# Performance work log

Measured on AMD Instinct MI355X. Metric: run time of the kernel, lower is better.

The kernel has to match this reference:

```python
import jax, jax.numpy as jnp
import numpy as np

H = 1024
VOCAB = 32000


def setup_inputs() -> dict:
    key = jax.random.key(0)
    ks = jax.random.split(key, 16)
    N, B, T = 32, 64, 400
    s = 1.0 / np.sqrt(H)
    inp = {
        "input_seq": jax.random.randint(ks[0], (N, B), 0, VOCAB),
        "last_hidden": jax.random.normal(ks[1], (1, B, H), jnp.float32),
        "encoder_outputs": jax.random.normal(ks[2], (T, B, H), jnp.float32),
        "encoderB_outputs": jax.random.normal(ks[3], (T, B, H), jnp.float32),
        # parameters
        "emb": jax.random.normal(ks[4], (VOCAB, H), jnp.float32),
        "W_ih": jax.random.uniform(ks[5], (3 * H, H), jnp.float32, -s, s),
        "W_hh": jax.random.uniform(ks[6], (3 * H, H), jnp.float32, -s, s),
        "b_ih": jax.random.uniform(ks[7], (3 * H,), jnp.float32, -s, s),
        "b_hh": jax.random.uniform(ks[8], (3 * H,), jnp.float32, -s, s),
        "attn_W": jax.random.uniform(ks[9], (H, 2 * H), jnp.float32, -s, s),
        "attn_b": jax.random.uniform(ks[10], (H,), jnp.float32, -s, s),
        "attn_v": jax.random.uniform(ks[11], (H,), jnp.float32, -s, s),
        "concat_W": jax.random.uniform(ks[12], (H, 3 * H), jnp.float32, -s, s),
        "concat_b": jax.random.uniform(ks[13], (H,), jnp.float32, -s, s),
        "out_W": jax.random.uniform(ks[14], (VOCAB, H), jnp.float32, -s, s),
        "out_b": jax.random.uniform(ks[15], (VOCAB,), jnp.float32, -s, s),
    }
    return inp


def _gru(x, h0, W_ih, W_hh, b_ih, b_hh):
    # x: (N,B,H), h0: (B,H). PyTorch GRU cell equations.
    def step(h, x_t):
        gi = x_t @ W_ih.T + b_ih          # (B,3H)
        gh = h @ W_hh.T + b_hh
        i_r, i_z, i_n = jnp.split(gi, 3, axis=-1)
        h_r, h_z, h_n = jnp.split(gh, 3, axis=-1)
        r = jax.nn.sigmoid(i_r + h_r)
        z = jax.nn.sigmoid(i_z + h_z)
        n = jnp.tanh(i_n + r * h_n)
        h_new = (1.0 - z) * n + z * h
        return h_new, h_new
    hN, outs = jax.lax.scan(step, h0, x)
    return outs, hN


def _attention(rnn_out, enc, attn_W, attn_b, v):
    # score(h, e) = (Linear([h; e]) ) . v  -- linear in both, so separable.
    W1, W2 = attn_W[:, :H], attn_W[:, H:]
    u1 = W1.T @ v                         # (H,)
    u2 = W2.T @ v
    bias = attn_b @ v                     # scalar
    a = rnn_out @ u1                      # (N,B)
    c = enc @ u2 + bias                   # (T,B)
    # energies (B,N,T), softmax over T (matches F.softmax on (-1, max_len))
    e = a.T[:, :, None] + c.T[:, None, :]
    w = jax.nn.softmax(e, axis=-1)        # (B,N,T)
    ctx = jnp.einsum('bnt,tbh->nbh', w, enc)  # bmm then transpose(0,1)
    return w, ctx


def reference(input_seq, last_hidden, encoder_outputs, encoderB_outputs,
              emb, W_ih, W_hh, b_ih, b_hh, attn_W, attn_b, attn_v,
              concat_W, concat_b, out_W, out_b):
    x = emb[input_seq]                                   # (N,B,H)
    rnn_out, hN = _gru(x, last_hidden[0], W_ih, W_hh, b_ih, b_hh)
    hidden = hN[None]                                    # (1,B,H)
    uw, u_ctx = _attention(rnn_out, encoder_outputs, attn_W, attn_b, attn_v)
    bw, b_ctx = _attention(rnn_out, encoderB_outputs, attn_W, attn_b, attn_v)
    cat = jnp.concatenate([rnn_out, u_ctx, b_ctx], axis=2)   # (N,B,3H)
    h = jnp.tanh(cat @ concat_W.T + concat_b)
    output = h @ out_W.T + out_b                          # (N,B,VOCAB)
    return output, hidden, uw, bw
```

## Files before the change

kernel.cpp:

```cpp
#include <hip/hip_runtime.h>
#include <cstdint>
#include <cstddef>

namespace {

constexpr int kH  = 1024;
constexpr int kB  = 64;
constexpr int kN  = 32;
constexpr int kT  = 400;
constexpr int kV  = 32000;
constexpr int kM  = kN * kB;
constexpr int k3H = 3 * kH;

typedef _Float16 f16;
typedef _Float16 f16x4 __attribute__((ext_vector_type(4)));
typedef _Float16 f16x8 __attribute__((ext_vector_type(8)));
typedef float    f32x4v __attribute__((ext_vector_type(4)));

__device__ __forceinline__ void gload_lds16(const void* g, void* l) {
  __builtin_amdgcn_global_load_lds((__attribute__((address_space(1))) void*)g,
                                   (__attribute__((address_space(3))) void*)l,
                                   16, 0, 0);
}

__device__ __forceinline__ uint32_t pack_f16x2(f16 lo, f16 hi) {
  union { f16 h[2]; uint32_t u; } c;
  c.h[0] = lo; c.h[1] = hi;
  return c.u;
}


__global__ __launch_bounds__(256)
void pre_kernel(const float* __restrict__ Wih, f16* __restrict__ WihH,
                const float* __restrict__ Whh, f16* __restrict__ WhhH,
                const int* __restrict__ seq, const float* __restrict__ emb,
                f16* __restrict__ Xh, const float* __restrict__ lh,
                f16* __restrict__ HH0,
                const float* __restrict__ attnW, const float* __restrict__ attnB,
                const float* __restrict__ attnV,
                float* __restrict__ u2, float* __restrict__ biasS) {
  const int bid = blockIdx.x, tid = threadIdx.x;
  if (bid < 512) {
    const float* src = (bid < 256) ? Wih : Whh;
    f16* dst = (bid < 256) ? WihH : WhhH;
    constexpr int n4 = k3H * kH / 4;
    for (int i = (bid & 255) * 256 + tid; i < n4; i += 256 * 256) {
      float4 v = reinterpret_cast<const float4*>(src)[i];
      f16x4 o = { (f16)v.x, (f16)v.y, (f16)v.z, (f16)v.w };
      reinterpret_cast<f16x4*>(dst)[i] = o;
    }
  } else if (bid < 640) {
    const int m0 = (bid - 512) * 16;
    for (int k = 0; k < 16; ++k) {
      const int m = m0 + k;
      const int tok = seq[m];
      float4 v = reinterpret_cast<const float4*>(emb + (size_t)tok * kH)[tid];
      f16x4 o = { (f16)v.x, (f16)v.y, (f16)v.z, (f16)v.w };
      reinterpret_cast<f16x4*>(Xh + (size_t)m * kH)[tid] = o;
    }
  } else if (bid < 644) {
    for (int i = (bid - 640) * 256 + tid; i < 16384; i += 1024) {
      float4 v = reinterpret_cast<const float4*>(lh)[i];
      f16x4 o = { (f16)v.x, (f16)v.y, (f16)v.z, (f16)v.w };
      reinterpret_cast<f16x4*>(HH0)[i] = o;
    }
  } else {
    const int item = (bid - 644) * 4 + (tid >> 6);
    const int lane = tid & 63;
    if (item > kH) return;
    float sum = 0.0f;
    if (item < kH) {
      for (int k = lane; k < kH; k += 64)
        sum += attnW[(size_t)k * (2 * kH) + kH + item] * attnV[k];
    } else {
      for (int k = lane; k < kH; k += 64)
        sum += attnB[k] * attnV[k];
    }
    #pragma unroll
    for (int o = 32; o > 0; o >>= 1) sum += __shfl_xor(sum, o);
    if (lane == 0) { if (item < kH) u2[item] = sum; else biasS[0] = sum; }
  }
}


template <int MODE, typename OUT_T>
__global__ __launch_bounds__(256)
void gemm_bt2_kernel(const f16* __restrict__ A, const f16* __restrict__ Bt,
                     const float* __restrict__ bias, OUT_T* __restrict__ C,
                     int M, int N, int K) {
  __shared__ union {
    struct { __align__(16) f16 As[128 * 64]; __align__(16) f16 Bs[128 * 64]; } st;
    float rp32[64][132];
    f16   rp16[128][132];
  } sm;
  int bx, by;
  if (MODE == 2) {
    const int nrow = M >> 7;
    const int cpx  = gridDim.x >> 3;
    const int wgid = (blockIdx.x & 7) * cpx + (blockIdx.x >> 3);
    bx = wgid % nrow;  by = wgid / nrow;
  } else {
    bx = blockIdx.x;  by = blockIdx.y;
  }
  const int tid  = threadIdx.x;
  const int wave = tid >> 6;
  const int lane = tid & 63;
  const int m0 = bx * 128;
  const int n0 = by * 128;
  const int wm = (wave >> 1) * 64;
  const int wn = (wave & 1) * 64;
  const int rsub = lane >> 3;
  const int coff = (lane & 7) * 8;
  f32x4v acc[4][4] = {};
  const int nk = K >> 6;
  for (int kc = 0; kc < nk; ++kc) {
    const f16* Ag = A + (size_t)m0 * K + kc * 64;
    const f16* Bg = Bt + (size_t)n0 * K + kc * 64;
    for (int c = wave; c < 16; c += 4) {
      const int row = c * 8 + rsub;
      gload_lds16(Ag + (size_t)row * K + coff, &sm.st.As[c * 512]);
      gload_lds16(Bg + (size_t)row * K + coff, &sm.st.Bs[c * 512]);
    }
    __syncthreads();
    #pragma unroll
    for (int kk = 0; kk < 2; ++kk) {
      const int ko = kk * 32 + (lane >> 4) * 8;
      f16x8 af[4], bfr[4];
      #pragma unroll
      for (int i = 0; i < 4; ++i) {
        af[i]  = *reinterpret_cast<const f16x8*>(&sm.st.As[(wm + i * 16 + (lane & 15)) * 64 + ko]);
        bfr[i] = *reinterpret_cast<const f16x8*>(&sm.st.Bs[(wn + i * 16 + (lane & 15)) * 64 + ko]);
      }
      #pragma unroll
      for (int mi = 0; mi < 4; ++mi)
        #pragma unroll
        for (int ni = 0; ni < 4; ++ni)
          acc[mi][ni] = __builtin_amdgcn_mfma_f32_16x16x32_f16(af[mi], bfr[ni], acc[mi][ni], 0, 0, 0);
    }
    __syncthreads();
  }
  const int rb = (lane >> 4) * 4;
  const int cb = lane & 15;

  if (MODE == 1) {
    #pragma unroll
    for (int mi = 0; mi < 4; ++mi)
      #pragma unroll
      for (int ni = 0; ni < 4; ++ni) {
        const int col = wn + ni * 16 + cb;
        const float bv = bias[n0 + col];
        #pragma unroll
        for (int r = 0; r < 4; ++r)
          sm.rp16[wm + mi * 16 + rb + r][col] = (f16)tanhf(acc[mi][ni][r] + bv);
      }
    __syncthreads();
    #pragma unroll
    for (int i = 0; i < 8; ++i) {
      const int idx = i * 256 + tid;
      const int row = idx >> 4;
      const int c8  = (idx & 15) * 8;
      f16x8 v = *reinterpret_cast<const f16x8*>(&sm.rp16[row][c8]);
      *reinterpret_cast<f16x8*>(&C[(size_t)(m0 + row) * N + n0 + c8]) = v;
    }
  } else {
    #pragma unroll
    for (int half = 0; half < 2; ++half) {
      __syncthreads();
      if ((wm >> 6) == half) {
        #pragma unroll
        for (int mi = 0; mi < 4; ++mi)
          #pragma unroll
          for (int ni = 0; ni < 4; ++ni) {
            const int col = wn + ni * 16 + cb;
            const float bv = bias[n0 + col];
            #pragma unroll
            for (int r = 0; r < 4; ++r)
              sm.rp32[mi * 16 + rb + r][col] = acc[mi][ni][r] + bv;
          }
      }
      __syncthreads();
      #pragma unroll
      for (int i = 0; i < 8; ++i) {
        const int idx = i * 256 + tid;
        const int row = idx >> 5;
        const int c4  = (idx & 31) * 4;
        f32x4v v = *reinterpret_cast<const f32x4v*>(&sm.rp32[row][c4]);
        float* dst = (float*)&C[(size_t)(m0 + half * 64 + row) * N + n0 + c4];
        if (MODE == 2) __builtin_nontemporal_store(v, reinterpret_cast<f32x4v*>(dst));
        else *reinterpret_cast<f32x4v*>(dst) = v;
      }
    }
  }
}


constexpr int kGruBlks = 64;
constexpr int kAttnBlks = 128;
constexpr int kCvtBlks = 320;
constexpr int kMegaBlks = kGruBlks + kAttnBlks + kCvtBlks;

__global__ __launch_bounds__(256, 1)
void mega_kernel(const f16* __restrict__ Whh, const float* __restrict__ bhh,
                 const float* __restrict__ gi, const float* __restrict__ lh,
                 f16* __restrict__ HHa, f16* __restrict__ HHb,
                 f16* __restrict__ cath, float* __restrict__ hiddenOut,
                 unsigned int* __restrict__ flags,
                 const float* __restrict__ enc0, const float* __restrict__ enc1,
                 const float* __restrict__ u2, const float* __restrict__ biasS,
                 float* __restrict__ uw, float* __restrict__ bw,
                 const float* __restrict__ oW, f16* __restrict__ oWh,
                 const float* __restrict__ cW, f16* __restrict__ cWh) {
  __shared__ union SM {
    float ghp[4][64][52];
    struct { float4 u2s[256]; float srow[kT]; float red[8]; } at;
  } sm;
  const int bid = blockIdx.x;
  const int tid = threadIdx.x;
  const int wave = tid >> 6;
  const int lane = tid & 63;

  if (bid < kGruBlks) {
    const int ln   = lane & 15;
    const int khi  = lane >> 4;
    const int j0   = bid * 16;
    const int kw   = wave * 256;
    const int fm   = tid >> 2;
    const int fc   = (tid & 3) * 4;
    const int myprod = wave * 16 + ln;

    f16x8 bfr[3][8];
    #pragma unroll
    for (int s = 0; s < 3; ++s)
      #pragma unroll
      for (int ks = 0; ks < 8; ++ks)
        bfr[s][ks] = *reinterpret_cast<const f16x8*>(
            &Whh[(size_t)(s * kH + j0 + ln) * kH + kw + ks * 32 + khi * 8]);

    float hreg[4], bR[4], bZ[4], bN[4];
    #pragma unroll
    for (int e = 0; e < 4; ++e) {
      const int j = j0 + fc + e;
      hreg[e] = lh[(size_t)fm * kH + j];
      bR[e] = bhh[j]; bZ[e] = bhh[kH + j]; bN[e] = bhh[2 * kH + j];
    }

    for (int step = 0; step < kN; ++step) {
      const f16* hh  = (step & 1) ? HHb : HHa;
      f16*       hho = (step & 1) ? HHa : HHb;

      float4 giL[3];
      {
        const size_t mm = (size_t)step * kB + fm;
        #pragma unroll
        for (int s = 0; s < 3; ++s)
          giL[s] = *reinterpret_cast<const float4*>(&gi[mm * k3H + s * kH + j0 + fc]);
      }

      if (step > 0) {
        while (true) {
          unsigned int f = __hip_atomic_load(&flags[myprod], __ATOMIC_RELAXED,
                                             __HIP_MEMORY_SCOPE_SYSTEM);
          if (__all(f >= (unsigned int)step)) break;
          __builtin_amdgcn_s_sleep(1);
        }
        __builtin_amdgcn_fence(__ATOMIC_ACQUIRE, "agent");
      }

      f16x8 af[8][4];
      #pragma unroll
      for (int ks = 0; ks < 8; ++ks)
        #pragma unroll
        for (int mi = 0; mi < 4; ++mi)
          af[ks][mi] = *reinterpret_cast<const f16x8*>(
              &hh[(size_t)(mi * 16 + ln) * kH + kw + ks * 32 + khi * 8]);

      f32x4v acc[4][3] = {};
      #pragma unroll
      for (int ks = 0; ks < 8; ++ks)
        #pragma unroll
        for (int mi = 0; mi < 4; ++mi)
          #pragma unroll
          for (int s = 0; s < 3; ++s)
            acc[mi][s] = __builtin_amdgcn_mfma_f32_16x16x32_f16(af[ks][mi], bfr[s][ks], acc[mi][s], 0, 0, 0);

      #pragma unroll
      for (int mi = 0; mi < 4; ++mi)
        #pragma unroll
        for (int s = 0; s < 3; ++s)
          #pragma unroll
          for (int r = 0; r < 4; ++r)
            sm.ghp[wave][mi * 16 + khi * 4 + r][s * 16 + ln] = acc[mi][s][r];
      __syncthreads();

      float4 gr4 = {0,0,0,0}, gz4 = {0,0,0,0}, gn4 = {0,0,0,0};
      #pragma unroll
      for (int w = 0; w < 4; ++w) {
        float4 a = *reinterpret_cast<const float4*>(&sm.ghp[w][fm][fc]);
        float4 b = *reinterpret_cast<const float4*>(&sm.ghp[w][fm][16 + fc]);
        float4 c = *reinterpret_cast<const float4*>(&sm.ghp[w][fm][32 + fc]);
        gr4.x += a.x; gr4.y += a.y; gr4.z += a.z; gr4.w += a.w;
        gz4.x += b.x; gz4.y += b.y; gz4.z += b.z; gz4.w += b.w;
        gn4.x += c.x; gn4.y += c.y; gn4.z += c.z; gn4.w += c.w;
      }
      float hv[4];
      const float* grp = &gr4.x; const float* gzp = &gz4.x; const float* gnp = &gn4.x;
      const float* g0 = &giL[0].x; const float* g1 = &giL[1].x; const float* g2 = &giL[2].x;
      #pragma unroll
      for (int e = 0; e < 4; ++e) {
        const float r  = 1.0f / (1.0f + expf(-(g0[e] + grp[e] + bR[e])));
        const float z  = 1.0f / (1.0f + expf(-(g1[e] + gzp[e] + bZ[e])));
        const float nn = tanhf(g2[e] + r * (gnp[e] + bN[e]));
        hv[e] = (1.0f - z) * nn + z * hreg[e];
        hreg[e] = hv[e];
      }
      const uint32_t p01 = pack_f16x2((f16)hv[0], (f16)hv[1]);
      const uint32_t p23 = pack_f16x2((f16)hv[2], (f16)hv[3]);
      const unsigned long long pk64 = (unsigned long long)p01 | ((unsigned long long)p23 << 32);
      __hip_atomic_store(reinterpret_cast<unsigned long long*>(&hho[(size_t)fm * kH + j0 + fc]),
                         pk64, __ATOMIC_RELAXED, __HIP_MEMORY_SCOPE_AGENT);
      __syncthreads();
      if (step < kN - 1 && tid == 0)
        __hip_atomic_store(&flags[bid], (unsigned int)(step + 1),
                           __ATOMIC_RELAXED, __HIP_MEMORY_SCOPE_SYSTEM);
      uint2 pku; pku.x = p01; pku.y = p23;
      *reinterpret_cast<uint2*>(&cath[((size_t)step * kB + fm) * k3H + j0 + fc]) = pku;
      if (step == kN - 1) {
        float4 hv4 = { hv[0], hv[1], hv[2], hv[3] };
        *reinterpret_cast<float4*>(&hiddenOut[(size_t)fm * kH + j0 + fc]) = hv4;
      }
    }
  } else if (bid < kGruBlks + kAttnBlks) {
    const int idx = bid - kGruBlks;
    const int e = idx >> 6, b = idx & 63;
    const float* enc = e ? enc1 : enc0;

    sm.at.u2s[tid] = *reinterpret_cast<const float4*>(&u2[tid * 4]);
    __syncthreads();
    const float bias = biasS[0];

    for (int t = wave; t < kT; t += 4) {
      const float* row = enc + ((size_t)t * kB + b) * kH + lane * 16;
      float s = 0.0f;
      #pragma unroll
      for (int i = 0; i < 4; ++i) {
        float4 ev = reinterpret_cast<const float4*>(row)[i];
        float4 uv = sm.at.u2s[lane * 4 + i];
        s += ev.x * uv.x + ev.y * uv.y + ev.z * uv.z + ev.w * uv.w;
      }
      #pragma unroll
      for (int o = 32; o > 0; o >>= 1) s += __shfl_xor(s, o);
      if (lane == 0) sm.at.srow[t] = s + bias;
    }
    __syncthreads();

    float lmax = -1e30f;
    for (int t = tid; t < kT; t += 256) lmax = fmaxf(lmax, sm.at.srow[t]);
    #pragma unroll
    for (int o = 32; o > 0; o >>= 1) lmax = fmaxf(lmax, __shfl_xor(lmax, o));
    if (lane == 0) sm.at.red[wave] = lmax;
    __syncthreads();
    const float m = fmaxf(fmaxf(sm.at.red[0], sm.at.red[1]), fmaxf(sm.at.red[2], sm.at.red[3]));
    float lsum = 0.0f;
    for (int t = tid; t < kT; t += 256) {
      float ev = expf(sm.at.srow[t] - m);
      sm.at.srow[t] = ev;
      lsum += ev;
    }
    #pragma unroll
    for (int o = 32; o > 0; o >>= 1) lsum += __shfl_xor(lsum, o);
    if (lane == 0) sm.at.red[4 + wave] = lsum;
    __syncthreads();
    const float inv = 1.0f / (sm.at.red[4] + sm.at.red[5] + sm.at.red[6] + sm.at.red[7]);
    for (int t = tid; t < kT; t += 256) sm.at.srow[t] *= inv;
    __syncthreads();

    float* outp = (e ? bw : uw) + (size_t)b * kN * kT;
    for (int n = 0; n < kN; ++n)
      for (int t = tid; t < kT; t += 256)
        __builtin_nontemporal_store(sm.at.srow[t], &outp[n * kT + t]);

    const int j = tid * 4;
    float4 acc = {0,0,0,0};
    for (int t = 0; t < kT; ++t) {
      const float wt = sm.at.srow[t];
      const float4 ev = *reinterpret_cast<const float4*>(&enc[((size_t)t * kB + b) * kH + j]);
      acc.x += wt * ev.x; acc.y += wt * ev.y; acc.z += wt * ev.z; acc.w += wt * ev.w;
    }
    f16x4 cv = { (f16)acc.x, (f16)acc.y, (f16)acc.z, (f16)acc.w };
    #pragma unroll
    for (int n = 0; n < kN; ++n)
      *reinterpret_cast<f16x4*>(&cath[((size_t)(n * kB + b)) * k3H + kH + e * kH + j]) = cv;
  } else {
    constexpr int nOW = kV * kH / 4;
    constexpr int nCW = kH * k3H / 4;
    const int stride = kCvtBlks * 256;
    for (int i = (bid - kGruBlks - kAttnBlks) * 256 + tid; i < nOW + nCW; i += stride) {
      if (i < nOW) {
        float4 v = reinterpret_cast<const float4*>(oW)[i];
        f16x4 o = { (f16)v.x, (f16)v.y, (f16)v.z, (f16)v.w };
        reinterpret_cast<f16x4*>(oWh)[i] = o;
      } else {
        const int k = i - nOW;
        float4 v = reinterpret_cast<const float4*>(cW)[k];
        f16x4 o = { (f16)v.x, (f16)v.y, (f16)v.z, (f16)v.w };
        reinterpret_cast<f16x4*>(cWh)[k] = o;
      }
    }
  }
}

}


extern "C" void kernel_launch(void* const* d_in, const int* in_sizes, int n_in,
                              void* d_out, int out_size, void* d_ws, size_t ws_size,
                              hipStream_t stream) {
  (void)in_sizes; (void)n_in; (void)out_size; (void)ws_size;
  const int*   seq    = (const int*)d_in[0];
  const float* lh     = (const float*)d_in[1];
  const float* enc0   = (const float*)d_in[2];
  const float* enc1   = (const float*)d_in[3];
  const float* emb    = (const float*)d_in[4];
  const float* W_ih   = (const float*)d_in[5];
  const float* W_hh   = (const float*)d_in[6];
  const float* b_ih   = (const float*)d_in[7];
  const float* b_hh   = (const float*)d_in[8];
  const float* attn_W = (const float*)d_in[9];
  const float* attn_b = (const float*)d_in[10];
  const float* attn_v = (const float*)d_in[11];
  const float* cW     = (const float*)d_in[12];
  const float* cb     = (const float*)d_in[13];
  const float* oW     = (const float*)d_in[14];
  const float* ob     = (const float*)d_in[15];
  float* out = (float*)d_out;

  char* ws = (char*)d_ws;
  constexpr size_t oWih = 0;
  constexpr size_t oWhh = oWih + 6291456;
  constexpr size_t oCW  = oWhh + 6291456;
  constexpr size_t oOW  = oCW + 6291456;
  constexpr size_t oX   = oOW + 65536000;
  constexpr size_t oGI  = oX + 4194304;
  constexpr size_t oHH0 = oGI + 25165824;
  constexpr size_t oHH1 = oHH0 + 131072;
  constexpr size_t oCAT = oHH1 + 131072;
  constexpr size_t oH2  = oCAT + 12582912;
  constexpr size_t oU2  = oH2 + 4194304;
  constexpr size_t oBS  = oU2 + 4096;
  constexpr size_t oCTR = oBS + 256;

  f16*   Wih_h = (f16*)(ws + oWih);
  f16*   Whh_h = (f16*)(ws + oWhh);
  f16*   cW_h  = (f16*)(ws + oCW);
  f16*   oW_h  = (f16*)(ws + oOW);
  f16*   X_h   = (f16*)(ws + oX);
  float* GI    = (float*)(ws + oGI);
  f16*   HH0   = (f16*)(ws + oHH0);
  f16*   HH1   = (f16*)(ws + oHH1);
  f16*   CAT   = (f16*)(ws + oCAT);
  f16*   H2    = (f16*)(ws + oH2);
  float* U2    = (float*)(ws + oU2);
  float* BS    = (float*)(ws + oBS);
  unsigned int* FLAGS = (unsigned int*)(ws + oCTR);

  constexpr size_t oHidden = (size_t)kM * kV;
  constexpr size_t oUW = oHidden + (size_t)kB * kH;
  constexpr size_t oBW = oUW + (size_t)kB * kN * kT;

  pre_kernel<<<901, 256, 0, stream>>>(W_ih, Wih_h, W_hh, Whh_h, seq, emb, X_h,
                                      lh, HH0, attn_W, attn_b, attn_v, U2, BS);
  (void)hipMemsetAsync(FLAGS, 0, 64 * sizeof(unsigned int), stream);

  gemm_bt2_kernel<0, float><<<dim3(16, 24), 256, 0, stream>>>(X_h, Wih_h, b_ih, GI, kM, k3H, kH);

  mega_kernel<<<kMegaBlks, 256, 0, stream>>>(Whh_h, b_hh, GI, lh, HH0, HH1, CAT,
                                             out + oHidden, FLAGS,
                                             enc0, enc1, U2, BS,
                                             out + oUW, out + oBW,
                                             oW, oW_h, cW, cW_h);

  gemm_bt2_kernel<1, f16><<<dim3(16, 8), 256, 0, stream>>>(CAT, cW_h, cb, H2, kM, kH, k3H);
  gemm_bt2_kernel<2, float><<<4000, 256, 0, stream>>>(H2, oW_h, ob, out, kM, kV, kH);
}
```

Measured before the change: 715.6 us.

## Use 256x256 double-buffered swizzled GEMM for vocab projection

Replaces the 128x128 output-projection GEMM with a 512-thread 256x256 tile kernel. It double-buffers LDS with an XOR swizzle, interleaves prefetch of the next k-tile with MFMA phases, and raises wave priority around the MFMAs. The larger tile gives more operand reuse per LDS load and the pipeline hides global latency. In exchange, the LDS-staged coalesced epilogue and nontemporal stores are dropped for direct scattered stores, in both the new kernel and the smaller GEMMs. That may hurt write efficiency on the large 2048x32000 fp32 output.

Result: no change. 703.8 us (-1.7%).

```diff
diff --git a/kernel.cpp b/kernel.cpp
--- a/kernel.cpp
+++ b/kernel.cpp
@@ -83,30 +83,18 @@
 }
 
 
-template <int MODE, typename OUT_T>
+template <bool TANH, typename OUT_T>
 __global__ __launch_bounds__(256)
-void gemm_bt2_kernel(const f16* __restrict__ A, const f16* __restrict__ Bt,
-                     const float* __restrict__ bias, OUT_T* __restrict__ C,
-                     int M, int N, int K) {
-  __shared__ union {
-    struct { __align__(16) f16 As[128 * 64]; __align__(16) f16 Bs[128 * 64]; } st;
-    float rp32[64][132];
-    f16   rp16[128][132];
-  } sm;
-  int bx, by;
-  if (MODE == 2) {
-    const int nrow = M >> 7;
-    const int cpx  = gridDim.x >> 3;
-    const int wgid = (blockIdx.x & 7) * cpx + (blockIdx.x >> 3);
-    bx = wgid % nrow;  by = wgid / nrow;
-  } else {
-    bx = blockIdx.x;  by = blockIdx.y;
-  }
+void gemm_bt_kernel(const f16* __restrict__ A, const f16* __restrict__ Bt,
+                    const float* __restrict__ bias, OUT_T* __restrict__ C,
+                    int M, int N, int K) {
+  __shared__ __align__(16) f16 As[128 * 64];
+  __shared__ __align__(16) f16 Bs[128 * 64];
   const int tid  = threadIdx.x;
   const int wave = tid >> 6;
   const int lane = tid & 63;
-  const int m0 = bx * 128;
-  const int n0 = by * 128;
+  const int m0 = blockIdx.x * 128;
+  const int n0 = blockIdx.y * 128;
   const int wm = (wave >> 1) * 64;
   const int wn = (wave & 1) * 64;
   const int rsub = lane >> 3;
@@ -118,8 +106,8 @@
     const f16* Bg = Bt + (size_t)n0 * K + kc * 64;
     for (int c = wave; c < 16; c += 4) {
       const int row = c * 8 + rsub;
-      gload_lds16(Ag + (size_t)row * K + coff, &sm.st.As[c * 512]);
-      gload_lds16(Bg + (size_t)row * K + coff, &sm.st.Bs[c * 512]);
+      gload_lds16(Ag + (size_t)row * K + coff, &As[c * 512]);
+      gload_lds16(Bg + (size_t)row * K + coff, &Bs[c * 512]);
     }
     __syncthreads();
     #pragma unroll
@@ -128,8 +116,8 @@
       f16x8 af[4], bfr[4];
       #pragma unroll
       for (int i = 0; i < 4; ++i) {
-        af[i]  = *reinterpret_cast<const f16x8*>(&sm.st.As[(wm + i * 16 + (lane & 15)) * 64 + ko]);
-        bfr[i] = *reinterpret_cast<const f16x8*>(&sm.st.Bs[(wn + i * 16 + (lane & 15)) * 64 + ko]);
+        af[i]  = *reinterpret_cast<const f16x8*>(&As[(wm + i * 16 + (lane & 15)) * 64 + ko]);
+        bfr[i] = *reinterpret_cast<const f16x8*>(&Bs[(wn + i * 16 + (lane & 15)) * 64 + ko]);
       }
       #pragma unroll
       for (int mi = 0; mi < 4; ++mi)
@@ -141,56 +129,116 @@
   }
   const int rb = (lane >> 4) * 4;
   const int cb = lane & 15;
-
-  if (MODE == 1) {
-    #pragma unroll
-    for (int mi = 0; mi < 4; ++mi)
-      #pragma unroll
-      for (int ni = 0; ni < 4; ++ni) {
-        const int col = wn + ni * 16 + cb;
-        const float bv = bias[n0 + col];
-        #pragma unroll
-        for (int r = 0; r < 4; ++r)
-          sm.rp16[wm + mi * 16 + rb + r][col] = (f16)tanhf(acc[mi][ni][r] + bv);
-      }
-    __syncthreads();
-    #pragma unroll
-    for (int i = 0; i < 8; ++i) {
-      const int idx = i * 256 + tid;
-      const int row = idx >> 4;
-      const int c8  = (idx & 15) * 8;
-      f16x8 v = *reinterpret_cast<const f16x8*>(&sm.rp16[row][c8]);
-      *reinterpret_cast<f16x8*>(&C[(size_t)(m0 + row) * N + n0 + c8]) = v;
-    }
-  } else {
-    #pragma unroll
-    for (int half = 0; half < 2; ++half) {
-      __syncthreads();
-      if ((wm >> 6) == half) {
-        #pragma unroll
-        for (int mi = 0; mi < 4; ++mi)
+  #pragma unroll
+  for (int mi = 0; mi < 4; ++mi) {
+    #pragma unroll
+    for (int ni = 0; ni < 4; ++ni) {
+      const int col = n0 + wn + ni * 16 + cb;
+      const float bv = bias[col];
+      #pragma unroll
+      for (int r = 0; r < 4; ++r) {
+        const int row = m0 + wm + mi * 16 + rb + r;
+        float v = acc[mi][ni][r] + bv;
+        if (TANH) v = tanhf(v);
+        C[(size_t)row * N + col] = (OUT_T)v;
+      }
+    }
+  }
+}
+
+
+__global__ __launch_bounds__(512, 1)
+void gemm256_kernel(const f16* __restrict__ A, const f16* __restrict__ Bt,
+                    const float* __restrict__ bias, float* __restrict__ C) {
+  __shared__ __align__(16) f16 Abuf[2][256 * 64];
+  __shared__ __align__(16) f16 Bbuf[2][256 * 64];
+  const int tid  = threadIdx.x;
+  const int wave = tid >> 6;
+  const int lane = tid & 63;
+  const int ln15 = lane & 15;
+  const int khi  = lane >> 4;
+  const int l8   = lane >> 3;
+  const int cg   = (lane & 7) ^ l8;
+  const int xorE = (lane & 7) * 8;
+  const int wgid = (blockIdx.x & 7) * 125 + (blockIdx.x >> 3);
+  const int m0 = (wgid % 8) * 256;
+  const int n0 = (wgid / 8) * 256;
+  const int wm = (wave >> 2) * 128;
+  const int wn = (wave & 3) * 64;
+
+  auto stage_unit = [&](int kt, int u) {
+    const int half = u & 1;
+    f16* lb = (u & 2) ? &Bbuf[kt & 1][0] : &Abuf[kt & 1][0];
+    const f16* g = (u & 2) ? Bt : A;
+    const int g0 = (u & 2) ? n0 : m0;
+    #pragma unroll
+    for (int r = 0; r < 2; ++r) {
+      const int row = half * 128 + r * 64 + wave * 8;
+      gload_lds16(g + (size_t)(g0 + row + l8) * 1024 + kt * 64 + cg * 8,
+                  lb + row * 64);
+    }
+  };
+
+  f32x4v acc[8][4] = {};
+
+  stage_unit(0, 0); stage_unit(0, 1); stage_unit(0, 2); stage_unit(0, 3);
+  asm volatile("s_waitcnt vmcnt(0)" ::: "memory");
+  __builtin_amdgcn_s_barrier();
+  asm volatile("" ::: "memory");
+
+  for (int kt = 0; kt < 16; ++kt) {
+    const f16* Ab = &Abuf[kt & 1][0];
+    const f16* Bb = &Bbuf[kt & 1][0];
+    #pragma unroll
+    for (int p = 0; p < 4; ++p) {
+      if (kt < 15) {
+        if (p == 0) { stage_unit(kt + 1, 0); stage_unit(kt + 1, 1); }
+        else if (p == 1) stage_unit(kt + 1, 2);
+        else if (p == 2) stage_unit(kt + 1, 3);
+      }
+      f16x8 af[2][2], bf[4][2];
+      #pragma unroll
+      for (int kk = 0; kk < 2; ++kk) {
+        const int kox = (kk * 32 + khi * 8) ^ xorE;
+        #pragma unroll
+        for (int i = 0; i < 2; ++i)
+          af[i][kk] = *reinterpret_cast<const f16x8*>(
+              &Ab[(wm + (2 * p + i) * 16 + ln15) * 64 + kox]);
+        #pragma unroll
+        for (int n = 0; n < 4; ++n)
+          bf[n][kk] = *reinterpret_cast<const f16x8*>(
+              &Bb[(wn + n * 16 + ln15) * 64 + kox]);
+      }
+      __builtin_amdgcn_s_setprio(1);
+      #pragma unroll
+      for (int kk = 0; kk < 2; ++kk)
+        #pragma unroll
+        for (int i = 0; i < 2; ++i)
           #pragma unroll
-          for (int ni = 0; ni < 4; ++ni) {
-            const int col = wn + ni * 16 + cb;
-            const float bv = bias[n0 + col];
-            #pragma unroll
-            for (int r = 0; r < 4; ++r)
-              sm.rp32[mi * 16 + rb + r][col] = acc[mi][ni][r] + bv;
-          }
-      }
-      __syncthreads();
-      #pragma unroll
-      for (int i = 0; i < 8; ++i) {
-        const int idx = i * 256 + tid;
-        const int row = idx >> 5;
-        const int c4  = (idx & 31) * 4;
-        f32x4v v = *reinterpret_cast<const f32x4v*>(&sm.rp32[row][c4]);
-        float* dst = (float*)&C[(size_t)(m0 + half * 64 + row) * N + n0 + c4];
-        if (MODE == 2) __builtin_nontemporal_store(v, reinterpret_cast<f32x4v*>(dst));
-        else *reinterpret_cast<f32x4v*>(dst) = v;
+          for (int n = 0; n < 4; ++n)
+            acc[2 * p + i][n] = __builtin_amdgcn_mfma_f32_16x16x32_f16(
+                af[i][kk], bf[n][kk], acc[2 * p + i][n], 0, 0, 0);
+      __builtin_amdgcn_s_setprio(0);
+      if (p == 3) {
+        asm volatile("s_waitcnt vmcnt(0)" ::: "memory");
+        __builtin_amdgcn_s_barrier();
+        asm volatile("" ::: "memory");
+      } else {
+        __builtin_amdgcn_s_barrier();
       }
     }
   }
+
+  #pragma unroll
+  for (int mf = 0; mf < 8; ++mf)
+    #pragma unroll
+    for (int n = 0; n < 4; ++n) {
+      const int col = n0 + wn + n * 16 + ln15;
+      const float bv = bias[col];
+      #pragma unroll
+      for (int r = 0; r < 4; ++r)
+        C[(size_t)(m0 + wm + mf * 16 + khi * 4 + r) * kV + col] = acc[mf][n][r] + bv;
+    }
 }
 
 
@@ -471,7 +519,7 @@
                                       lh, HH0, attn_W, attn_b, attn_v, U2, BS);
   (void)hipMemsetAsync(FLAGS, 0, 64 * sizeof(unsigned int), stream);
 
-  gemm_bt2_kernel<0, float><<<dim3(16, 24), 256, 0, stream>>>(X_h, Wih_h, b_ih, GI, kM, k3H, kH);
+  gemm_bt_kernel<false, float><<<dim3(16, 24), 256, 0, stream>>>(X_h, Wih_h, b_ih, GI, kM, k3H, kH);
 
   mega_kernel<<<kMegaBlks, 256, 0, stream>>>(Whh_h, b_hh, GI, lh, HH0, HH1, CAT,
                                              out + oHidden, FLAGS,
@@ -479,6 +527,6 @@
                                              out + oUW, out + oBW,
                                              oW, oW_h, cW, cW_h);
 
-  gemm_bt2_kernel<1, f16><<<dim3(16, 8), 256, 0, stream>>>(CAT, cW_h, cb, H2, kM, kH, k3H);
-  gemm_bt2_kernel<2, float><<<4000, 256, 0, stream>>>(H2, oW_h, ob, out, kM, kV, kH);
-}
+  gemm_bt_kernel<true, f16><<<dim3(16, 8), 256, 0, stream>>>(CAT, cW_h, cb, H2, kM, kH, k3H);
+  gemm256_kernel<<<1000, 512, 0, stream>>>(H2, oW_h, ob, out);
+}
```
